# Optimization experiments

Measured on AMD Instinct MI355X. Metric: run time of the kernel, lower is better.

Reference implementation:

```python
import jax, jax.numpy as jnp
import numpy as np

N = 12000   # num_node
D = 128     # hiddenSize
HID = 256   # hidden_channels
B = 512     # batch
L = 20      # citing history length
F = 400     # title_vec + journal_vec
FF = 512    # transformer dim_feedforward
NH = 4      # heads
STDV = float(1.0 / np.sqrt(D))


def _unif(k, shape):
    return jax.random.uniform(k, shape, jnp.float32, -STDV, STDV)


def setup_inputs():
    key = jax.random.key(0)
    ks = jax.random.split(key, 40)
    inp = {}
    inp['embedding'] = _unif(ks[0], (N, D))
    inp['f1_w'] = _unif(ks[1], (D, F)); inp['f1_b'] = _unif(ks[2], (D,))
    # two GNN modules, each a 2-layer GCN (assumed structure)
    inp['gcn0_w1'] = _unif(ks[3], (D, HID)); inp['gcn0_b1'] = _unif(ks[4], (HID,))
    inp['gcn0_w2'] = _unif(ks[5], (HID, D)); inp['gcn0_b2'] = _unif(ks[6], (D,))
    inp['gcn1_w1'] = _unif(ks[7], (D, HID)); inp['gcn1_b1'] = _unif(ks[8], (HID,))
    inp['gcn1_w2'] = _unif(ks[9], (HID, D)); inp['gcn1_b2'] = _unif(ks[10], (D,))
    # transformer encoder layer (post-norm, relu), reset_parameters makes ALL weights uniform
    inp['in_proj_w'] = _unif(ks[11], (3 * D, D)); inp['in_proj_b'] = _unif(ks[12], (3 * D,))
    inp['out_proj_w'] = _unif(ks[13], (D, D)); inp['out_proj_b'] = _unif(ks[14], (D,))
    inp['ln1_s'] = _unif(ks[15], (D,)); inp['ln1_b'] = _unif(ks[16], (D,))
    inp['ff1_w'] = _unif(ks[17], (FF, D)); inp['ff1_b'] = _unif(ks[18], (FF,))
    inp['ff2_w'] = _unif(ks[19], (D, FF)); inp['ff2_b'] = _unif(ks[20], (D,))
    inp['ln2_s'] = _unif(ks[21], (D,)); inp['ln2_b'] = _unif(ks[22], (D,))
    # forward inputs
    inp['adj_mat'] = jax.random.uniform(ks[23], (N, N), jnp.float32) * (2.0 / N)  # ~row-stochastic
    inp['node_feature'] = jax.random.normal(ks[24], (N, F), jnp.float32)
    inp['H_content'] = jax.random.normal(ks[25], (B, 10), jnp.float32)  # unused in forward
    inp['citing'] = jax.random.randint(ks[26], (B,), 0, N)
    inp['h_items'] = jax.random.randint(ks[27], (B,), 0, N)  # unused in forward
    inp['u_seqs'] = jax.random.randint(ks[28], (B, L), 0, N)
    inp['u_seqs_num'] = jax.random.randint(ks[29], (B,), 1, L)  # unused in forward
    return inp


def _layer_norm(x, s, b):
    m = x.mean(-1, keepdims=True)
    v = ((x - m) ** 2).mean(-1, keepdims=True)
    return (x - m) * jax.lax.rsqrt(v + 1e-5) * s + b


def reference(embedding, f1_w, f1_b,
              gcn0_w1, gcn0_b1, gcn0_w2, gcn0_b2,
              gcn1_w1, gcn1_b1, gcn1_w2, gcn1_b2,
              in_proj_w, in_proj_b, out_proj_w, out_proj_b,
              ln1_s, ln1_b, ff1_w, ff1_b, ff2_w, ff2_b, ln2_s, ln2_b,
              adj_mat, node_feature, H_content,
              citing, h_items, u_seqs, u_seqs_num):
    # embedding gate
    nf = node_feature @ f1_w.T + f1_b          # [N, D]
    x = embedding * nf                          # [N, D]
    # GCN stack: each GNN = relu((A x) W1 + b1) -> (A h) W2 + b2
    for (w1, b1, w2, b2) in ((gcn0_w1, gcn0_b1, gcn0_w2, gcn0_b2),
                             (gcn1_w1, gcn1_b1, gcn1_w2, gcn1_b2)):
        h = jax.nn.relu((adj_mat @ x) @ w1 + b1)
        x = (adj_mat @ h) @ w2 + b2
    item = x                                    # [N, D]
    seq = item[u_seqs]                          # [B, L, D]
    # torch TransformerEncoderLayer with batch_first=False: dim0 (B) is the
    # sequence axis, dim1 (L) is the batch axis (faithful to original code).
    qkv = seq @ in_proj_w.T + in_proj_b         # [B, L, 3D]
    q, k, v = jnp.split(qkv, 3, axis=-1)
    dh = D // NH
    q = q.reshape(B, L, NH, dh) * (1.0 / np.sqrt(dh))
    k = k.reshape(B, L, NH, dh)
    v = v.reshape(B, L, NH, dh)
    att = jax.nn.softmax(jnp.einsum('snhd,tnhd->nhst', q, k), axis=-1)  # attn over seq axis s,t=B
    o = jnp.einsum('nhst,tnhd->snhd', att, v).reshape(B, L, D)
    o = o @ out_proj_w.T + out_proj_b
    x1 = _layer_norm(seq + o, ln1_s, ln1_b)
    ff = jax.nn.relu(x1 @ ff1_w.T + ff1_b) @ ff2_w.T + ff2_b
    x2 = _layer_norm(x1 + ff, ln2_s, ln2_b)
    citing_vec = x2.mean(axis=1)                # mean over dim=1 (L), [B, D]
    citing_feats = nf[citing]                   # [B, D]
    citing_paper = jnp.concatenate([citing_vec, citing_feats], axis=1)  # [B, 2D]
    cited_paper = jnp.concatenate([item, nf], axis=1)                   # [N, 2D]
    scores = citing_paper @ cited_paper.T       # [B, N]
    return scores
```

## Files before the change

kernel.cpp:

```cpp
#include <hip/hip_runtime.h>
#include <hip/hip_bf16.h>

typedef __hip_bfloat16 bf;
typedef __attribute__((ext_vector_type(4))) float f32x4;
typedef __attribute__((ext_vector_type(8))) __bf16 bf16x8;
typedef __attribute__((ext_vector_type(8))) short short8;

#define NN 12000
#define DD 128
#define HIDC 256
#define BBATCH 512
#define LSEQ 20
#define FFEAT 400
#define FFDIM 512
#define AZ 5
#define AKS (NN / AZ)

__device__ __forceinline__ float b2f(bf v) { return __bfloat162float(v); }
__device__ __forceinline__ bf f2b(float v) { return __float2bfloat16(v); }
__device__ __forceinline__ float us2f(unsigned short u) {
    return __uint_as_float(((unsigned int)u) << 16);
}
__device__ __forceinline__ unsigned short f2us(float f) {
    bf h = __float2bfloat16(f);
    return __builtin_bit_cast(unsigned short, h);
}

__device__ __forceinline__ void gload_lds16(const bf* g, bf* l) {
    __builtin_amdgcn_global_load_lds(
        (__attribute__((address_space(1))) void*)(g),
        (__attribute__((address_space(3))) void*)(l),
        16, 0, 0);
}

template<bool F32>
__device__ __forceinline__ short8 ld8(const void* p, long long idx) {
    if (F32) {
        const float* fp = (const float*)p + idx;
        f32x4 u0 = *(const f32x4*)fp;
        f32x4 u1 = *(const f32x4*)(fp + 4);
        short8 s;
        s[0] = (short)f2us(u0[0]); s[1] = (short)f2us(u0[1]);
        s[2] = (short)f2us(u0[2]); s[3] = (short)f2us(u0[3]);
        s[4] = (short)f2us(u1[0]); s[5] = (short)f2us(u1[1]);
        s[6] = (short)f2us(u1[2]); s[7] = (short)f2us(u1[3]);
        return s;
    } else {
        return *(const short8*)((const bf*)p + idx);
    }
}

template<bool F32>
__device__ __forceinline__ bf ldelem(const void* p, long long idx) {
    if (F32) return f2b(((const float*)p)[idx]);
    return ((const bf*)p)[idx];
}

__global__ __launch_bounds__(512) void adj_gemm8(
    const bf* __restrict__ A,
    const bf* __restrict__ Bt,
    float* __restrict__ part)
{
    alignas(16) __shared__ bf As[4][128 * 64];
    alignas(16) __shared__ bf Bs[4][128 * 64];
    const int tid = threadIdx.x;
    const int lane = tid & 63;
    const int w = tid >> 6;
    const int z = blockIdx.y;
    const long long k0 = (long long)z * AKS;
    int m0 = blockIdx.x * 128;
    if (m0 > NN - 128) m0 = NN - 128;

    const int rowi = lane >> 3;
    const int chks = (lane & 7) ^ rowi;
    const bf* gA[2]; const bf* gB[2]; int lo[2];
    #pragma unroll
    for (int i = 0; i < 2; i++) {
        int rbase = 16 * w + 8 * i;
        gA[i] = A  + (long long)(m0 + rbase + rowi) * NN + k0 + chks * 8;
        gB[i] = Bt + (long long)(rbase + rowi) * NN + k0 + chks * 8;
        lo[i] = rbase * 64;
    }
    const int rowiT = lane >> 2;
    const int chksT = (lane & 3) ^ ((lane >> 3) & 3);
    const bf* gAT = A  + (long long)(m0 + 16 * w + rowiT) * NN + k0 + 2368 + chksT * 8;
    const bf* gBT = Bt + (long long)(16 * w + rowiT) * NN + k0 + 2368 + chksT * 8;
    const int loT = (16 * w) * 32;

    const int wr = (w >> 1) * 32, wc = (w & 1) * 64;
    const int fr = lane & 15;
    const int kq = lane >> 4;
    int aoff[2][2], boff[2][4], aoffT[2], boffT[4];
    #pragma unroll
    for (int mi = 0; mi < 2; mi++) {
        int ra = wr + mi * 16 + fr;
        aoff[0][mi] = ra * 64 + ((kq)     ^ (ra & 7)) * 8;
        aoff[1][mi] = ra * 64 + ((4 + kq) ^ (ra & 7)) * 8;
        aoffT[mi]   = ra * 32 + (kq ^ ((ra >> 1) & 3)) * 8;
    }
    #pragma unroll
    for (int ni = 0; ni < 4; ni++) {
        int rb = wc + ni * 16 + fr;
        boff[0][ni] = rb * 64 + ((kq)     ^ (rb & 7)) * 8;
        boff[1][ni] = rb * 64 + ((4 + kq) ^ (rb & 7)) * 8;
        boffT[ni]   = rb * 32 + (kq ^ ((rb >> 1) & 3)) * 8;
    }
    f32x4 acc[2][4] = {};

    auto stage64 = [&](int t, int b) {
        const long long go = (long long)t * 64;
        const int bo = b * (128 * 64);
        #pragma unroll
        for (int i = 0; i < 2; i++) {
            gload_lds16(gA[i] + go, &As[0][0] + bo + lo[i]);
            gload_lds16(gB[i] + go, &Bs[0][0] + bo + lo[i]);
        }
    };
    auto stageTail = [&]() {
        gload_lds16(gAT, &As[1][0] + loT);
        gload_lds16(gBT, &Bs[1][0] + loT);
    };
    auto compute64 = [&](int b) {
        const bf* Ab = &As[0][0] + b * (128 * 64);
        const bf* Bb = &Bs[0][0] + b * (128 * 64);
        #pragma unroll
        for (int s = 0; s < 2; s++) {
            bf16x8 af[2], bfr[4];
            #pragma unroll
            for (int mi = 0; mi < 2; mi++) af[mi]  = *(const bf16x8*)(Ab + aoff[s][mi]);
            #pragma unroll
            for (int ni = 0; ni < 4; ni++) bfr[ni] = *(const bf16x8*)(Bb + boff[s][ni]);
            #pragma unroll
            for (int mi = 0; mi < 2; mi++)
                #pragma unroll
                for (int ni = 0; ni < 4; ni++)
                    acc[mi][ni] = __builtin_amdgcn_mfma_f32_16x16x32_bf16(
                        af[mi], bfr[ni], acc[mi][ni], 0, 0, 0);
        }
    };

    stage64(0, 0);
    stage64(1, 1);
    stage64(2, 2);

    #pragma unroll 1
    for (int t = 0; t < 35; t++) {
        asm volatile("s_waitcnt vmcnt(8)" ::: "memory");
        __builtin_amdgcn_s_barrier();
        __builtin_amdgcn_sched_barrier(0);
        compute64(t & 3);
        if (t < 34) stage64(t + 3, (t + 3) & 3);
        else        stageTail();
    }
    asm volatile("s_waitcnt vmcnt(6)" ::: "memory");
    __builtin_amdgcn_s_barrier();
    __builtin_amdgcn_sched_barrier(0);
    compute64(3);
    asm volatile("s_waitcnt vmcnt(2)" ::: "memory");
    __builtin_amdgcn_s_barrier();
    __builtin_amdgcn_sched_barrier(0);
    compute64(0);
    asm volatile("s_waitcnt vmcnt(0)" ::: "memory");
    __builtin_amdgcn_s_barrier();
    __builtin_amdgcn_sched_barrier(0);
    {
        bf16x8 af[2], bfr[4];
        #pragma unroll
        for (int mi = 0; mi < 2; mi++) af[mi]  = *(const bf16x8*)(&As[1][0] + aoffT[mi]);
        #pragma unroll
        for (int ni = 0; ni < 4; ni++) bfr[ni] = *(const bf16x8*)(&Bs[1][0] + boffT[ni]);
        #pragma unroll
        for (int mi = 0; mi < 2; mi++)
            #pragma unroll
            for (int ni = 0; ni < 4; ni++)
                acc[mi][ni] = __builtin_amdgcn_mfma_f32_16x16x32_bf16(
                    af[mi], bfr[ni], acc[mi][ni], 0, 0, 0);
    }

    float* C = part + (long long)z * ((long long)NN * 128);
    const int cr0 = (lane >> 4) * 4;
    const int cc = lane & 15;
    #pragma unroll
    for (int mi = 0; mi < 2; mi++) {
        #pragma unroll
        for (int ni = 0; ni < 4; ni++) {
            int col = wc + ni * 16 + cc;
            #pragma unroll
            for (int j = 0; j < 4; j++) {
                int row = m0 + wr + mi * 16 + cr0 + j;
                C[(long long)row * 128 + col] = acc[mi][ni][j];
            }
        }
    }
}

template<bool A_F32, bool B_F32, bool HAS_BIAS, bool RELU, bool OUT_F32, bool SIDE_A>
__global__ __launch_bounds__(256) void gemm128(
    const void* __restrict__ A, int lda, long long sA1, long long sA2,
    const void* __restrict__ Bm, int ldb, long long sB1, long long sB2,
    const float* __restrict__ bias,
    void* __restrict__ Cv, int ldc, long long sC1, long long sC2,
    int M, int N, int K, int tilesN, int zdiv, float alpha,
    bf* __restrict__ sideA)
{
    __shared__ bf As[128][40];
    __shared__ bf Bs[128][40];
    const int tid = threadIdx.x;
    const int z = blockIdx.y;
    const int zq = z / zdiv, zr = z - zq * zdiv;
    const char* Ap = (const char*)A;
    const char* Bp = (const char*)Bm;
    const long long offA = (long long)zq * sA1 + (long long)zr * sA2;
    const long long offB = (long long)zq * sB1 + (long long)zr * sB2;
    const long long offC = (long long)zq * sC1 + (long long)zr * sC2;
    const int tm = blockIdx.x / tilesN, tn = blockIdx.x - tm * tilesN;
    int m0 = tm * 128; if (m0 > M - 128) m0 = M - 128;
    const int n0 = tn * 128;
    const int lane = tid & 63;
    const int wv = tid >> 6;
    const int wr = (wv >> 1) * 64, wc = (wv & 1) * 64;
    const int fr = lane & 15;
    const int kq = (lane >> 4) * 8;
    const int sr = tid >> 2, scol = (tid & 3) * 8;
    f32x4 acc[4][4] = {};

    for (int k0 = 0; k0 < K; k0 += 32) {
        if (k0 + 32 <= K) {
            const long long ia0 = offA + (long long)(m0 + sr) * lda + k0 + scol;
            const long long ia1 = offA + (long long)(m0 + sr + 64) * lda + k0 + scol;
            short8 va0 = ld8<A_F32>(Ap, ia0);
            short8 va1 = ld8<A_F32>(Ap, ia1);
            short8 vb0 = {0,0,0,0,0,0,0,0}, vb1 = {0,0,0,0,0,0,0,0};
            if (n0 + sr < N)      vb0 = ld8<B_F32>(Bp, offB + (long long)(n0 + sr) * ldb + k0 + scol);
            if (n0 + sr + 64 < N) vb1 = ld8<B_F32>(Bp, offB + (long long)(n0 + sr + 64) * ldb + k0 + scol);
            if (SIDE_A) {
                *(short8*)&sideA[ia0] = va0;
                *(short8*)&sideA[ia1] = va1;
            }
            *(short8*)&As[sr][scol] = va0;
            *(short8*)&As[sr + 64][scol] = va1;
            *(short8*)&Bs[sr][scol] = vb0;
            *(short8*)&Bs[sr + 64][scol] = vb1;
        } else {
            bf zv = f2b(0.f);
            for (int i = tid; i < 128 * 32; i += 256) {
                int r = i >> 5, c = i & 31, gk = k0 + c;
                As[r][c] = (gk < K) ? ldelem<A_F32>(Ap, offA + (long long)(m0 + r) * lda + gk) : zv;
                Bs[r][c] = (gk < K && n0 + r < N) ? ldelem<B_F32>(Bp, offB + (long long)(n0 + r) * ldb + gk) : zv;
            }
        }
        __syncthreads();
        bf16x8 af[4], bfg[4];
        #pragma unroll
        for (int i = 0; i < 4; i++) af[i]  = *(const bf16x8*)&As[wr + i * 16 + fr][kq];
        #pragma unroll
        for (int i = 0; i < 4; i++) bfg[i] = *(const bf16x8*)&Bs[wc + i * 16 + fr][kq];
        #pragma unroll
        for (int mi = 0; mi < 4; mi++)
            #pragma unroll
            for (int ni = 0; ni < 4; ni++)
                acc[mi][ni] = __builtin_amdgcn_mfma_f32_16x16x32_bf16(
                    af[mi], bfg[ni], acc[mi][ni], 0, 0, 0);
        __syncthreads();
    }

    const int cr0 = (lane >> 4) * 4;
    const int cc = lane & 15;
    #pragma unroll
    for (int mi = 0; mi < 4; mi++) {
        #pragma unroll
        for (int ni = 0; ni < 4; ni++) {
            int col = n0 + wc + ni * 16 + cc;
            if (col >= N) continue;
            float bv = 0.f;
            if (HAS_BIAS) bv = bias[col];
            #pragma unroll
            for (int j = 0; j < 4; j++) {
                int row = m0 + wr + mi * 16 + cr0 + j;
                float v = acc[mi][ni][j] * alpha + bv;
                if (RELU) v = fmaxf(v, 0.f);
                if (OUT_F32) ((float*)Cv)[offC + (long long)row * ldc + col] = v;
                else ((bf*)Cv)[offC + (long long)row * ldc + col] = f2b(v);
            }
        }
    }
}

template<bool IN_F32>
__global__ __launch_bounds__(256) void transpose_k(
    const void* __restrict__ in, int ldin, long long sI1, long long sI2, int zdiv,
    const float* __restrict__ mulp, int ldmul,
    bf* __restrict__ outp, int ldout, long long sOut,
    int R, int C)
{
    __shared__ bf t[32][33];
    const int z = blockIdx.z;
    const int zq = z / zdiv, zr = z - zq * zdiv;
    const long long offI = (long long)zq * sI1 + (long long)zr * sI2;
    bf* op = outp + (long long)z * sOut;
    int r0 = blockIdx.x * 32, c0 = blockIdx.y * 32;
    int tx = threadIdx.x, ty = threadIdx.y;
    #pragma unroll
    for (int i = 0; i < 4; i++) {
        int r = r0 + ty + i * 8, c = c0 + tx;
        bf v = f2b(0.f);
        if (r < R && c < C) {
            v = ldelem<IN_F32>(in, offI + (long long)r * ldin + c);
            if (mulp) v = f2b(b2f(v) * mulp[(long long)r * ldmul + c]);
        }
        t[ty + i * 8][tx] = v;
    }
    __syncthreads();
    #pragma unroll
    for (int i = 0; i < 4; i++) {
        int c = c0 + ty + i * 8, r = r0 + tx;
        if (c < C && r < R) op[(long long)c * ldout + r] = t[tx][ty + i * 8];
    }
}

__global__ __launch_bounds__(256) void reduceK(
    const float* __restrict__ part, const float* __restrict__ bias,
    bf* __restrict__ outp, int total, int nz, long long zs)
{
    int i = blockIdx.x * 256 + threadIdx.x;
    if (i >= total) return;
    float s = 0.f;
    for (int zz = 0; zz < nz; zz++) s += part[(long long)zz * zs + i];
    if (bias) s += bias[i & 127];
    outp[i] = f2b(s);
}

__global__ __launch_bounds__(256) void gather_rows(
    const bf* __restrict__ src, const int* __restrict__ idx,
    bf* __restrict__ dst, int nrows)
{
    int t = blockIdx.x * 256 + threadIdx.x;
    int row = t >> 4, p = t & 15;
    if (row >= nrows) return;
    long long srow = idx[row];
    *(short8*)&dst[(long long)row * 128 + p * 8] =
        *(const short8*)&src[srow * 128 + p * 8];
}

__global__ __launch_bounds__(256) void softmax512(bf* __restrict__ S, int nrows)
{
    int gid = blockIdx.x * 256 + threadIdx.x;
    int wid = gid >> 6, lane = gid & 63;
    if (wid >= nrows) return;
    bf* row = S + (long long)wid * 512;
    short8 raw = *(const short8*)&row[lane * 8];
    float v[8];
    float mx = -3.0e38f;
    #pragma unroll
    for (int j = 0; j < 8; j++) {
        v[j] = us2f((unsigned short)raw[j]);
        mx = fmaxf(mx, v[j]);
    }
    #pragma unroll
    for (int off = 32; off; off >>= 1) mx = fmaxf(mx, __shfl_xor(mx, off, 64));
    float sum = 0.f;
    #pragma unroll
    for (int j = 0; j < 8; j++) { v[j] = __expf(v[j] - mx); sum += v[j]; }
    #pragma unroll
    for (int off = 32; off; off >>= 1) sum += __shfl_xor(sum, off, 64);
    float inv = 1.f / sum;
    short8 o;
    #pragma unroll
    for (int j = 0; j < 8; j++) o[j] = (short)f2us(v[j] * inv);
    *(short8*)&row[lane * 8] = o;
}

__global__ __launch_bounds__(256) void ln_rows(
    const bf* __restrict__ a, const bf* __restrict__ bres,
    const float* __restrict__ sc, const float* __restrict__ bi,
    bf* __restrict__ outp, int nrows)
{
    int gid = blockIdx.x * 256 + threadIdx.x;
    int wid = gid >> 6, lane = gid & 63;
    if (wid >= nrows) return;
    long long base = (long long)wid * 128;
    int i0 = lane * 2, i1 = lane * 2 + 1;
    float x0 = b2f(a[base + i0]) + b2f(bres[base + i0]);
    float x1 = b2f(a[base + i1]) + b2f(bres[base + i1]);
    float s = x0 + x1;
    #pragma unroll
    for (int off = 32; off; off >>= 1) s += __shfl_xor(s, off, 64);
    float mean = s * (1.f / 128.f);
    float d0 = x0 - mean, d1 = x1 - mean;
    float vv = d0 * d0 + d1 * d1;
    #pragma unroll
    for (int off = 32; off; off >>= 1) vv += __shfl_xor(vv, off, 64);
    float inv = rsqrtf(vv * (1.f / 128.f) + 1e-5f);
    outp[base + i0] = f2b(d0 * inv * sc[i0] + bi[i0]);
    outp[base + i1] = f2b(d1 * inv * sc[i1] + bi[i1]);
}

__global__ __launch_bounds__(256) void build_citing(
    const bf* __restrict__ x2, const bf* __restrict__ nf,
    const int* __restrict__ citing, bf* __restrict__ cp)
{
    int i = blockIdx.x * 256 + threadIdx.x;
    if (i >= BBATCH * 256) return;
    int b = i >> 8, d = i & 255;
    float v;
    if (d < 128) {
        float s = 0.f;
        for (int l = 0; l < LSEQ; l++)
            s += b2f(x2[((long long)b * LSEQ + l) * 128 + d]);
        v = s * (1.f / (float)LSEQ);
    } else {
        v = b2f(nf[(long long)citing[b] * 128 + (d - 128)]);
    }
    cp[i] = f2b(v);
}

__global__ __launch_bounds__(256) void build_cited(
    const bf* __restrict__ item, const bf* __restrict__ nf, bf* __restrict__ outp)
{
    int i = blockIdx.x * 256 + threadIdx.x;
    if (i >= NN * 256) return;
    int r = i >> 8, d = i & 255;
    outp[i] = (d < 128) ? item[(long long)r * 128 + d]
                        : nf[(long long)r * 128 + (d - 128)];
}

extern "C" void kernel_launch(void* const* d_in, const int* in_sizes, int n_in,
                              void* d_out, int out_size, void* d_ws, size_t ws_size,
                              hipStream_t stream)
{
    const float* emb  = (const float*)d_in[0];
    const float* f1w  = (const float*)d_in[1];
    const float* f1b  = (const float*)d_in[2];
    const float* g0w1 = (const float*)d_in[3];  const float* g0b1 = (const float*)d_in[4];
    const float* g0w2 = (const float*)d_in[5];  const float* g0b2 = (const float*)d_in[6];
    const float* g1w1 = (const float*)d_in[7];  const float* g1b1 = (const float*)d_in[8];
    const float* g1w2 = (const float*)d_in[9];  const float* g1b2 = (const float*)d_in[10];
    const float* ipw  = (const float*)d_in[11]; const float* ipb  = (const float*)d_in[12];
    const float* opw  = (const float*)d_in[13]; const float* opb  = (const float*)d_in[14];
    const float* ln1s = (const float*)d_in[15]; const float* ln1b = (const float*)d_in[16];
    const float* ff1w = (const float*)d_in[17]; const float* ff1b = (const float*)d_in[18];
    const float* ff2w = (const float*)d_in[19]; const float* ff2b = (const float*)d_in[20];
    const float* ln2s = (const float*)d_in[21]; const float* ln2b = (const float*)d_in[22];
    const float* adj  = (const float*)d_in[23];
    const float* nfe  = (const float*)d_in[24];
    const int* citing = (const int*)d_in[26];
    const int* useqs  = (const int*)d_in[28];
    float* outp = (float*)d_out;

    size_t off = 0;
    auto carve = [&](size_t bytes) -> char* {
        char* p = (char*)d_ws + off;
        off += (bytes + 255) & ~(size_t)255;
        return p;
    };
    bf* adjb = (bf*)carve((size_t)NN * NN * 2);
    bf* nf   = (bf*)carve((size_t)NN * DD * 2);
    bf* bufP = (bf*)carve((size_t)NN * DD * 2);
    bf* bufQ = (bf*)carve((size_t)NN * DD * 2);
    bf* BT   = (bf*)carve((size_t)NN * DD * 2);
    bf* Hbuf = (bf*)carve((size_t)NN * HIDC * 2);
    float* part = (float*)carve((size_t)AZ * NN * DD * 4);
    bf* seq  = (bf*)carve((size_t)10240 * DD * 2);
    bf* qkv  = (bf*)carve((size_t)10240 * 384 * 2);
    bf* Sb   = (bf*)carve((size_t)80 * 512 * 512 * 2);
    bf* w10T = (bf*)carve((size_t)DD * HIDC * 2);
    bf* w20T = (bf*)carve((size_t)DD * HIDC * 2);
    bf* w11T = (bf*)carve((size_t)DD * HIDC * 2);
    bf* w21T = (bf*)carve((size_t)DD * HIDC * 2);
    bf* x1ln = (bf*)Hbuf;
    bf* cp   = (bf*)((char*)Hbuf + (size_t)10240 * DD * 2);
    char* pr = (char*)part;
    bf* VT   = (bf*)pr; pr += (size_t)80 * 32 * 512 * 2;
    bf* o_   = (bf*)pr; pr += (size_t)10240 * DD * 2;
    bf* o2   = (bf*)pr; pr += (size_t)10240 * DD * 2;
    bf* ffh  = (bf*)pr; pr += (size_t)10240 * FFDIM * 2;
    bf* ff2o = (bf*)pr; pr += (size_t)10240 * DD * 2;
    bf* x2   = (bf*)pr; pr += (size_t)10240 * DD * 2;
    bf* cited= (bf*)pr; pr += (size_t)NN * 256 * 2;

    dim3 tb(256), tb512(512), tt(32, 8);
    const long long NM = (long long)NN * DD;

    transpose_k<true><<<dim3(4, 8, 1), tt, 0, stream>>>(g0w1, HIDC, 0, 0, 1, nullptr, 0, w10T, DD, 0, DD, HIDC);
    transpose_k<true><<<dim3(8, 4, 1), tt, 0, stream>>>(g0w2, DD, 0, 0, 1, nullptr, 0, w20T, HIDC, 0, HIDC, DD);
    transpose_k<true><<<dim3(4, 8, 1), tt, 0, stream>>>(g1w1, HIDC, 0, 0, 1, nullptr, 0, w11T, DD, 0, DD, HIDC);
    transpose_k<true><<<dim3(8, 4, 1), tt, 0, stream>>>(g1w2, DD, 0, 0, 1, nullptr, 0, w21T, HIDC, 0, HIDC, DD);

    gemm128<true, true, true, false, false, false><<<dim3(94, 1), tb, 0, stream>>>(
        nfe, FFEAT, 0, 0, f1w, FFEAT, 0, 0, f1b,
        nf, DD, 0, 0, NN, DD, FFEAT, 1, 1, 1.f, nullptr);
    transpose_k<false><<<dim3(375, 4, 1), tt, 0, stream>>>(nf, DD, 0, 0, 1, emb, DD, BT, NN, 0, NN, DD);

    const float* biases2[2] = { g0b2, g1b2 };
    const float* biases1[2] = { g0b1, g1b1 };
    const bf* w1T[2] = { w10T, w11T };
    const bf* w2T[2] = { w20T, w21T };
    bf* xout[2] = { bufP, bufQ };

    for (int g = 0; g < 2; g++) {
        if (g == 0) {
            gemm128<true, false, false, false, true, true><<<dim3(94, AZ), tb, 0, stream>>>(
                adj, NN, AKS, 0, BT, NN, AKS, 0, nullptr,
                part, DD, NM, 0, NN, DD, AKS, 1, 1, 1.f, adjb);
        } else {
            adj_gemm8<<<dim3(94, AZ), tb512, 0, stream>>>(adjb, BT, part);
        }
        bf* tbuf = (g == 0) ? bufP : bufQ;
        reduceK<<<dim3((NM + 255) / 256), tb, 0, stream>>>(part, nullptr, tbuf, (int)NM, AZ, NM);
        gemm128<false, false, true, true, false, false><<<dim3(188, 1), tb, 0, stream>>>(
            tbuf, DD, 0, 0, w1T[g], DD, 0, 0, biases1[g],
            Hbuf, HIDC, 0, 0, NN, HIDC, DD, 2, 1, 1.f, nullptr);
        bf* t2buf = (g == 0) ? bufQ : bufP;
        gemm128<false, false, false, false, false, false><<<dim3(94, 1), tb, 0, stream>>>(
            Hbuf, HIDC, 0, 0, w2T[g], HIDC, 0, 0, nullptr,
            t2buf, DD, 0, 0, NN, DD, HIDC, 1, 1, 1.f, nullptr);
        transpose_k<false><<<dim3(375, 4, 1), tt, 0, stream>>>(t2buf, DD, 0, 0, 1, nullptr, 0, BT, NN, 0, NN, DD);
        adj_gemm8<<<dim3(94, AZ), tb512, 0, stream>>>(adjb, BT, part);
        reduceK<<<dim3((NM + 255) / 256), tb, 0, stream>>>(part, biases2[g], xout[g], (int)NM, AZ, NM);
        if (g == 0) {
            transpose_k<false><<<dim3(375, 4, 1), tt, 0, stream>>>(bufP, DD, 0, 0, 1, nullptr, 0, BT, NN, 0, NN, DD);
        }
    }
    bf* item = bufQ;

    gather_rows<<<dim3(640), tb, 0, stream>>>(item, useqs, seq, 10240);
    gemm128<false, true, true, false, false, false><<<dim3(240, 1), tb, 0, stream>>>(
        seq, DD, 0, 0, ipw, DD, 0, 0, ipb,
        qkv, 384, 0, 0, 10240, 384, DD, 3, 1, 1.f, nullptr);
    transpose_k<false><<<dim3(16, 1, 80), tt, 0, stream>>>(
        qkv + 256, 7680, 384, 32, 4, nullptr, 0, VT, 512, 16384, 512, 32);
    gemm128<false, false, false, false, false, false><<<dim3(16, 80), tb, 0, stream>>>(
        qkv, 7680, 384, 32, qkv + 128, 7680, 384, 32, nullptr,
        Sb, 512, (long long)4 * 262144, 262144, 512, 512, 32, 4, 4, 0.17677669529663687f, nullptr);
    softmax512<<<dim3(10240), tb, 0, stream>>>(Sb, 80 * 512);
    gemm128<false, false, false, false, false, false><<<dim3(4, 80), tb, 0, stream>>>(
        Sb, 512, (long long)4 * 262144, 262144, VT, 512, (long long)4 * 16384, 16384, nullptr,
        o_, 2560, 128, 32, 512, 32, 512, 1, 4, 1.f, nullptr);
    gemm128<false, true, true, false, false, false><<<dim3(80, 1), tb, 0, stream>>>(
        o_, DD, 0, 0, opw, DD, 0, 0, opb,
        o2, DD, 0, 0, 10240, DD, DD, 1, 1, 1.f, nullptr);
    ln_rows<<<dim3(2560), tb, 0, stream>>>(seq, o2, ln1s, ln1b, x1ln, 10240);
    gemm128<false, true, true, true, false, false><<<dim3(320, 1), tb, 0, stream>>>(
        x1ln, DD, 0, 0, ff1w, DD, 0, 0, ff1b,
        ffh, FFDIM, 0, 0, 10240, FFDIM, DD, 4, 1, 1.f, nullptr);
    gemm128<false, true, true, false, false, false><<<dim3(80, 1), tb, 0, stream>>>(
        ffh, FFDIM, 0, 0, ff2w, FFDIM, 0, 0, ff2b,
        ff2o, DD, 0, 0, 10240, DD, FFDIM, 1, 1, 1.f, nullptr);
    ln_rows<<<dim3(2560), tb, 0, stream>>>(x1ln, ff2o, ln2s, ln2b, x2, 10240);
    build_citing<<<dim3(512), tb, 0, stream>>>(x2, nf, citing, cp);
    build_cited<<<dim3(12000), tb, 0, stream>>>(item, nf, cited);
    gemm128<false, false, false, false, true, false><<<dim3(376, 1), tb, 0, stream>>>(
        cp, 256, 0, 0, cited, 256, 0, 0, nullptr,
        outp, NN, 0, 0, BBATCH, NN, 256, 94, 1, 1.f, nullptr);
}
```

Measured before the change: 766.7 us.

## Fuse GEMM with residual LayerNorm, read cited halves directly, batch weight transposes

Adds a gemm_ln kernel that computes the out-projection and FF2 GEMMs with bias, residual add and LayerNorm in the epilogue. This removes two separate ln_rows passes and the intermediate o2/ff2o round trips. The scores GEMM now loads the item and nf halves directly instead of first building a concatenated cited matrix. Four tiny weight-transpose launches are merged into one. The fused LayerNorm uses an E[x^2]-mean^2 variance, which is slightly less numerically stable.

```diff
diff --git a/kernel.cpp b/kernel.cpp
--- a/kernel.cpp
+++ b/kernel.cpp
@@ -286,6 +286,206 @@
     }
 }
 
+__global__ __launch_bounds__(256) void gemm_ln(
+    const bf* __restrict__ A, int lda,
+    const float* __restrict__ Bw,
+    const float* __restrict__ bias,
+    const bf* __restrict__ resid,
+    const float* __restrict__ lnS, const float* __restrict__ lnB,
+    bf* __restrict__ outp, int K)
+{
+    __shared__ bf As[128][40];
+    __shared__ bf Bs[128][40];
+    __shared__ float red[128][2][2];
+    const int tid = threadIdx.x;
+    const int m0 = blockIdx.x * 128;
+    const int lane = tid & 63;
+    const int wv = tid >> 6;
+    const int wr = (wv >> 1) * 64, wc = (wv & 1) * 64;
+    const int fr = lane & 15;
+    const int kq = (lane >> 4) * 8;
+    const int sr = tid >> 2, scol = (tid & 3) * 8;
+    f32x4 acc[4][4] = {};
+
+    for (int k0 = 0; k0 < K; k0 += 32) {
+        short8 va0 = ld8<false>(A, (long long)(m0 + sr) * lda + k0 + scol);
+        short8 va1 = ld8<false>(A, (long long)(m0 + sr + 64) * lda + k0 + scol);
+        short8 vb0 = ld8<true>(Bw, (long long)sr * K + k0 + scol);
+        short8 vb1 = ld8<true>(Bw, (long long)(sr + 64) * K + k0 + scol);
+        *(short8*)&As[sr][scol] = va0;
+        *(short8*)&As[sr + 64][scol] = va1;
+        *(short8*)&Bs[sr][scol] = vb0;
+        *(short8*)&Bs[sr + 64][scol] = vb1;
+        __syncthreads();
+        bf16x8 af[4], bfg[4];
+        #pragma unroll
+        for (int i = 0; i < 4; i++) af[i]  = *(const bf16x8*)&As[wr + i * 16 + fr][kq];
+        #pragma unroll
+        for (int i = 0; i < 4; i++) bfg[i] = *(const bf16x8*)&Bs[wc + i * 16 + fr][kq];
+        #pragma unroll
+        for (int mi = 0; mi < 4; mi++)
+            #pragma unroll
+            for (int ni = 0; ni < 4; ni++)
+                acc[mi][ni] = __builtin_amdgcn_mfma_f32_16x16x32_bf16(
+                    af[mi], bfg[ni], acc[mi][ni], 0, 0, 0);
+        __syncthreads();
+    }
+
+    const int cr0 = (lane >> 4) * 4;
+    const int cc = lane & 15;
+    #pragma unroll
+    for (int mi = 0; mi < 4; mi++)
+        #pragma unroll
+        for (int ni = 0; ni < 4; ni++) {
+            int col = wc + ni * 16 + cc;
+            #pragma unroll
+            for (int j = 0; j < 4; j++) {
+                int row = m0 + wr + mi * 16 + cr0 + j;
+                acc[mi][ni][j] += bias[col] + b2f(resid[(long long)row * 128 + col]);
+            }
+        }
+    float s1[4][4], s2[4][4];
+    #pragma unroll
+    for (int mi = 0; mi < 4; mi++)
+        #pragma unroll
+        for (int j = 0; j < 4; j++) {
+            float a = 0.f, b = 0.f;
+            #pragma unroll
+            for (int ni = 0; ni < 4; ni++) {
+                float x = acc[mi][ni][j];
+                a += x; b += x * x;
+            }
+            #pragma unroll
+            for (int off = 1; off < 16; off <<= 1) {
+                a += __shfl_xor(a, off, 64);
+                b += __shfl_xor(b, off, 64);
+            }
+            s1[mi][j] = a; s2[mi][j] = b;
+        }
+    if (cc == 0) {
+        #pragma unroll
+        for (int mi = 0; mi < 4; mi++)
+            #pragma unroll
+            for (int j = 0; j < 4; j++) {
+                int lr = wr + mi * 16 + cr0 + j;
+                red[lr][wv & 1][0] = s1[mi][j];
+                red[lr][wv & 1][1] = s2[mi][j];
+            }
+    }
+    __syncthreads();
+    #pragma unroll
+    for (int mi = 0; mi < 4; mi++)
+        #pragma unroll
+        for (int ni = 0; ni < 4; ni++) {
+            int col = wc + ni * 16 + cc;
+            float ls = lnS[col], lb = lnB[col];
+            #pragma unroll
+            for (int j = 0; j < 4; j++) {
+                int lr = wr + mi * 16 + cr0 + j;
+                float tot  = red[lr][0][0] + red[lr][1][0];
+                float tot2 = red[lr][0][1] + red[lr][1][1];
+                float mean = tot * (1.f / 128.f);
+                float var  = tot2 * (1.f / 128.f) - mean * mean;
+                float inv  = rsqrtf(var + 1e-5f);
+                outp[(long long)(m0 + lr) * 128 + col] =
+                    f2b((acc[mi][ni][j] - mean) * inv * ls + lb);
+            }
+        }
+}
+
+__global__ __launch_bounds__(256) void gemm_scores(
+    const bf* __restrict__ A,
+    const bf* __restrict__ B1,
+    const bf* __restrict__ B2,
+    float* __restrict__ outp)
+{
+    __shared__ bf As[128][40];
+    __shared__ bf Bs[128][40];
+    const int tid = threadIdx.x;
+    const int tm = blockIdx.x / 94, tn = blockIdx.x - tm * 94;
+    const int m0 = tm * 128;
+    const int n0 = tn * 128;
+    const int lane = tid & 63;
+    const int wv = tid >> 6;
+    const int wr = (wv >> 1) * 64, wc = (wv & 1) * 64;
+    const int fr = lane & 15;
+    const int kq = (lane >> 4) * 8;
+    const int sr = tid >> 2, scol = (tid & 3) * 8;
+    f32x4 acc[4][4] = {};
+
+    for (int k0 = 0; k0 < 256; k0 += 32) {
+        short8 va0 = ld8<false>(A, (long long)(m0 + sr) * 256 + k0 + scol);
+        short8 va1 = ld8<false>(A, (long long)(m0 + sr + 64) * 256 + k0 + scol);
+        const int gk = k0 + scol;
+        const bf* bb = (gk < 128) ? B1 : B2;
+        const int kk = gk & 127;
+        short8 vb0 = {0,0,0,0,0,0,0,0}, vb1 = {0,0,0,0,0,0,0,0};
+        if (n0 + sr < NN)      vb0 = *(const short8*)(bb + (long long)(n0 + sr) * 128 + kk);
+        if (n0 + sr + 64 < NN) vb1 = *(const short8*)(bb + (long long)(n0 + sr + 64) * 128 + kk);
+        *(short8*)&As[sr][scol] = va0;
+        *(short8*)&As[sr + 64][scol] = va1;
+        *(short8*)&Bs[sr][scol] = vb0;
+        *(short8*)&Bs[sr + 64][scol] = vb1;
+        __syncthreads();
+        bf16x8 af[4], bfg[4];
+        #pragma unroll
+        for (int i = 0; i < 4; i++) af[i]  = *(const bf16x8*)&As[wr + i * 16 + fr][kq];
+        #pragma unroll
+        for (int i = 0; i < 4; i++) bfg[i] = *(const bf16x8*)&Bs[wc + i * 16 + fr][kq];
+        #pragma unroll
+        for (int mi = 0; mi < 4; mi++)
+            #pragma unroll
+            for (int ni = 0; ni < 4; ni++)
+                acc[mi][ni] = __builtin_amdgcn_mfma_f32_16x16x32_bf16(
+                    af[mi], bfg[ni], acc[mi][ni], 0, 0, 0);
+        __syncthreads();
+    }
+
+    const int cr0 = (lane >> 4) * 4;
+    const int cc = lane & 15;
+    #pragma unroll
+    for (int mi = 0; mi < 4; mi++) {
+        #pragma unroll
+        for (int ni = 0; ni < 4; ni++) {
+            int col = n0 + wc + ni * 16 + cc;
+            if (col >= NN) continue;
+            #pragma unroll
+            for (int j = 0; j < 4; j++) {
+                int row = m0 + wr + mi * 16 + cr0 + j;
+                outp[(long long)row * NN + col] = acc[mi][ni][j];
+            }
+        }
+    }
+}
+
+__global__ __launch_bounds__(256) void transpose4_k(
+    const float* s0, const float* s1, const float* s2, const float* s3,
+    bf* d0, bf* d1, bf* d2, bf* d3)
+{
+    __shared__ bf t[32][33];
+    const int z = blockIdx.z;
+    const float* in = (z == 0) ? s0 : (z == 1) ? s1 : (z == 2) ? s2 : s3;
+    bf* out = (z == 0) ? d0 : (z == 1) ? d1 : (z == 2) ? d2 : d3;
+    const int R = (z & 1) ? HIDC : DD;
+    const int C = (z & 1) ? DD : HIDC;
+    int r0 = blockIdx.x * 32, c0 = blockIdx.y * 32;
+    if (r0 >= R || c0 >= C) return;
+    int tx = threadIdx.x, ty = threadIdx.y;
+    #pragma unroll
+    for (int i = 0; i < 4; i++) {
+        int r = r0 + ty + i * 8, c = c0 + tx;
+        bf v = f2b(0.f);
+        if (r < R && c < C) v = f2b(in[(long long)r * C + c]);
+        t[ty + i * 8][tx] = v;
+    }
+    __syncthreads();
+    #pragma unroll
+    for (int i = 0; i < 4; i++) {
+        int c = c0 + ty + i * 8, r = r0 + tx;
+        if (c < C && r < R) out[(long long)c * R + r] = t[tx][ty + i * 8];
+    }
+}
+
 template<bool IN_F32>
 __global__ __launch_bounds__(256) void transpose_k(
     const void* __restrict__ in, int ldin, long long sI1, long long sI2, int zdiv,
@@ -368,31 +568,6 @@
     #pragma unroll
     for (int j = 0; j < 8; j++) o[j] = (short)f2us(v[j] * inv);
     *(short8*)&row[lane * 8] = o;
-}
-
-__global__ __launch_bounds__(256) void ln_rows(
-    const bf* __restrict__ a, const bf* __restrict__ bres,
-    const float* __restrict__ sc, const float* __restrict__ bi,
-    bf* __restrict__ outp, int nrows)
-{
-    int gid = blockIdx.x * 256 + threadIdx.x;
-    int wid = gid >> 6, lane = gid & 63;
-    if (wid >= nrows) return;
-    long long base = (long long)wid * 128;
-    int i0 = lane * 2, i1 = lane * 2 + 1;
-    float x0 = b2f(a[base + i0]) + b2f(bres[base + i0]);
-    float x1 = b2f(a[base + i1]) + b2f(bres[base + i1]);
-    float s = x0 + x1;
-    #pragma unroll
-    for (int off = 32; off; off >>= 1) s += __shfl_xor(s, off, 64);
-    float mean = s * (1.f / 128.f);
-    float d0 = x0 - mean, d1 = x1 - mean;
-    float vv = d0 * d0 + d1 * d1;
-    #pragma unroll
-    for (int off = 32; off; off >>= 1) vv += __shfl_xor(vv, off, 64);
-    float inv = rsqrtf(vv * (1.f / 128.f) + 1e-5f);
-    outp[base + i0] = f2b(d0 * inv * sc[i0] + bi[i0]);
-    outp[base + i1] = f2b(d1 * inv * sc[i1] + bi[i1]);
 }
 
 __global__ __launch_bounds__(256) void build_citing(
@@ -412,16 +587,6 @@
         v = b2f(nf[(long long)citing[b] * 128 + (d - 128)]);
     }
     cp[i] = f2b(v);
-}
-
-__global__ __launch_bounds__(256) void build_cited(
-    const bf* __restrict__ item, const bf* __restrict__ nf, bf* __restrict__ outp)
-{
-    int i = blockIdx.x * 256 + threadIdx.x;
-    if (i >= NN * 256) return;
-    int r = i >> 8, d = i & 255;
-    outp[i] = (d < 128) ? item[(long long)r * 128 + d]
-                        : nf[(long long)r * 128 + (d - 128)];
 }
 
 extern "C" void kernel_launch(void* const* d_in, const int* in_sizes, int n_in,
@@ -476,15 +641,12 @@
     bf* ffh  = (bf*)pr; pr += (size_t)10240 * FFDIM * 2;
     bf* ff2o = (bf*)pr; pr += (size_t)10240 * DD * 2;
     bf* x2   = (bf*)pr; pr += (size_t)10240 * DD * 2;
-    bf* cited= (bf*)pr; pr += (size_t)NN * 256 * 2;
 
     dim3 tb(256), tb512(512), tt(32, 8);
     const long long NM = (long long)NN * DD;
 
-    transpose_k<true><<<dim3(4, 8, 1), tt, 0, stream>>>(g0w1, HIDC, 0, 0, 1, nullptr, 0, w10T, DD, 0, DD, HIDC);
-    transpose_k<true><<<dim3(8, 4, 1), tt, 0, stream>>>(g0w2, DD, 0, 0, 1, nullptr, 0, w20T, HIDC, 0, HIDC, DD);
-    transpose_k<true><<<dim3(4, 8, 1), tt, 0, stream>>>(g1w1, HIDC, 0, 0, 1, nullptr, 0, w11T, DD, 0, DD, HIDC);
-    transpose_k<true><<<dim3(8, 4, 1), tt, 0, stream>>>(g1w2, DD, 0, 0, 1, nullptr, 0, w21T, HIDC, 0, HIDC, DD);
+    transpose4_k<<<dim3(8, 8, 4), tt, 0, stream>>>(
+        g0w1, g0w2, g1w1, g1w2, w10T, w20T, w11T, w21T);
 
     gemm128<true, true, true, false, false, false><<<dim3(94, 1), tb, 0, stream>>>(
         nfe, FFEAT, 0, 0, f1w, FFEAT, 0, 0, f1b,
@@ -536,20 +698,12 @@
     gemm128<false, false, false, false, false, false><<<dim3(4, 80), tb, 0, stream>>>(
         Sb, 512, (long long)4 * 262144, 262144, VT, 512, (long long)4 * 16384, 16384, nullptr,
         o_, 2560, 128, 32, 512, 32, 512, 1, 4, 1.f, nullptr);
-    gemm128<false, true, true, false, false, false><<<dim3(80, 1), tb, 0, stream>>>(
-        o_, DD, 0, 0, opw, DD, 0, 0, opb,
-        o2, DD, 0, 0, 10240, DD, DD, 1, 1, 1.f, nullptr);
-    ln_rows<<<dim3(2560), tb, 0, stream>>>(seq, o2, ln1s, ln1b, x1ln, 10240);
+    gemm_ln<<<dim3(80), tb, 0, stream>>>(o_, DD, opw, opb, seq, ln1s, ln1b, x1ln, DD);
     gemm128<false, true, true, true, false, false><<<dim3(320, 1), tb, 0, stream>>>(
         x1ln, DD, 0, 0, ff1w, DD, 0, 0, ff1b,
         ffh, FFDIM, 0, 0, 10240, FFDIM, DD, 4, 1, 1.f, nullptr);
-    gemm128<false, true, true, false, false, false><<<dim3(80, 1), tb, 0, stream>>>(
-        ffh, FFDIM, 0, 0, ff2w, FFDIM, 0, 0, ff2b,
-        ff2o, DD, 0, 0, 10240, DD, FFDIM, 1, 1, 1.f, nullptr);
-    ln_rows<<<dim3(2560), tb, 0, stream>>>(x1ln, ff2o, ln2s, ln2b, x2, 10240);
+    gemm_ln<<<dim3(80), tb, 0, stream>>>(ffh, FFDIM, ff2w, ff2b, x1ln, ln2s, ln2b, x2, FFDIM);
     build_citing<<<dim3(512), tb, 0, stream>>>(x2, nf, citing, cp);
-    build_cited<<<dim3(12000), tb, 0, stream>>>(item, nf, cited);
-    gemm128<false, false, false, false, true, false><<<dim3(376, 1), tb, 0, stream>>>(
-        cp, 256, 0, 0, cited, 256, 0, 0, nullptr,
-        outp, NN, 0, 0, BBATCH, NN, 256, 94, 1, 1.f, nullptr);
-}
+    gemm_scores<<<dim3(376), tb, 0, stream>>>(cp, item, nf, outp);
+    (void)o2; (void)ff2o;
+}
```

New measurement: 735.9 us. 1.04x faster.
